# Kernel optimization log

Hardware: AMD Instinct MI355X
Metric: run time of the kernel (lower is better)

The kernel has to match this reference:

```python
import jax, jax.numpy as jnp
import numpy as np

N = 100000       # nodes
DEG = 16         # in-degree per node
E = N * DEG      # edges
IN_DIM = 128
H_DIM = 128
NEG_SLOPE = 0.01  # F.leaky_relu default


def setup_inputs() -> dict:
    key = jax.random.key(0)
    ks = jax.random.split(key, 12)
    sc = 0.05
    attr = jax.random.normal(ks[0], (N, IN_DIM), jnp.float32)
    edge_d = jax.random.uniform(ks[1], (E, 1), dtype=jnp.float32)
    edge_src = jax.random.randint(ks[2], (E,), 0, N, dtype=jnp.int32)
    edge_dst = jnp.repeat(jnp.arange(N, dtype=jnp.int32), DEG)  # every node gets DEG msgs
    return {
        "attr": attr,
        "edge_d": edge_d,
        "W_V1": jax.random.normal(ks[3], (1, 1), jnp.float32) * sc,
        "W_W1": jax.random.normal(ks[4], (H_DIM, IN_DIM), jnp.float32) * sc,
        "W_U1": jax.random.normal(ks[5], (H_DIM, IN_DIM), jnp.float32) * sc,
        "W_a1": jax.random.normal(ks[6], (1, 2 * H_DIM + 1), jnp.float32) * sc,
        "W_V2": jax.random.normal(ks[7], (1, 1), jnp.float32) * sc,
        "W_W2": jax.random.normal(ks[8], (H_DIM, H_DIM), jnp.float32) * sc,
        "W_U2": jax.random.normal(ks[9], (H_DIM, H_DIM), jnp.float32) * sc,
        "W_a2": jax.random.normal(ks[10], (1, 2 * H_DIM + 1), jnp.float32) * sc,
        "edge_src": edge_src,
        "edge_dst": edge_dst,
    }


def gat_layer(h, edge_d, edge_src, edge_dst, W_V, W_W, W_U, W_a):
    n = h.shape[0]
    t = edge_d @ W_V.T                      # [E,1] edge feature transform (fcV)
    z = h @ W_W.T                           # [N,H] (fcW)
    z_i = h @ W_U.T                         # [N,H] (fcU)
    Hd = z.shape[1]
    a = W_a[0]                              # [2H+1]
    a_src, a_dst, a_t = a[:Hd], a[Hd:2 * Hd], a[2 * Hd:]
    # attn_fc(concat(z_src, z_dst, t)) decomposed into per-node scores + edge term
    s_src = z @ a_src                       # [N]
    s_dst = z @ a_dst                       # [N]
    e = s_src[edge_src] + s_dst[edge_dst] + (t @ a_t)  # [E]
    e = jax.nn.leaky_relu(e, NEG_SLOPE)
    # per-destination-node softmax over incoming edges (mailbox softmax)
    m = jax.ops.segment_max(e, edge_dst, num_segments=n)
    ex = jnp.exp(e - m[edge_dst])
    denom = jax.ops.segment_sum(ex, edge_dst, num_segments=n)
    alpha = ex / denom[edge_dst]            # [E]
    # weighted neighbor aggregation
    zn = jax.ops.segment_sum(alpha[:, None] * z[edge_src], edge_dst, num_segments=n)
    return jax.nn.relu(z_i + zn)


def reference(attr, edge_d, W_V1, W_W1, W_U1, W_a1, W_V2, W_W2, W_U2, W_a2,
              edge_src, edge_dst):
    h = gat_layer(attr, edge_d, edge_src, edge_dst, W_V1, W_W1, W_U1, W_a1)
    h = gat_layer(h, edge_d, edge_src, edge_dst, W_V2, W_W2, W_U2, W_a2)
    return h
```

## Files before the change

### kernel.cpp

```cpp
#include <hip/hip_runtime.h>

#define N_NODES 100000
#define DEG 16
#define DIM 128
#define E_EDGES 1600000
#define NTILES 1563
#define T8 196
#define DGRID (T8 * 4 * 8)
#define LSTR 136

typedef short bf16x8 __attribute__((ext_vector_type(8)));
typedef float f32x4 __attribute__((ext_vector_type(4)));

__device__ __forceinline__ unsigned short f2bf(float f) {
    unsigned int u = __builtin_bit_cast(unsigned int, f);
    u = (u + 0x7fffu + ((u >> 16) & 1u)) >> 16;
    return (unsigned short)u;
}
__device__ __forceinline__ float bf2f(unsigned short h) {
    unsigned int u = ((unsigned int)h) << 16;
    return __builtin_bit_cast(float, u);
}
__device__ __forceinline__ bf16x8 pack_bf16x8(float4 lo, float4 hi) {
    bf16x8 f;
    f[0] = (short)f2bf(lo.x); f[1] = (short)f2bf(lo.y);
    f[2] = (short)f2bf(lo.z); f[3] = (short)f2bf(lo.w);
    f[4] = (short)f2bf(hi.x); f[5] = (short)f2bf(hi.y);
    f[6] = (short)f2bf(hi.z); f[7] = (short)f2bf(hi.w);
    return f;
}

__global__ __launch_bounds__(256) void prep_w(
    const float* __restrict__ W_W1, const float* __restrict__ W_U1,
    const float* __restrict__ W_W2, const float* __restrict__ W_U2,
    unsigned short* __restrict__ Wc1, unsigned short* __restrict__ Wc2)
{
    int idx = blockIdx.x * 256 + threadIdx.x;
    int half = idx & 32767;
    const float* src = (idx < 32768)
        ? (half < 16384 ? W_W1 + half : W_U1 + half - 16384)
        : (half < 16384 ? W_W2 + half : W_U2 + half - 16384);
    unsigned short* dst = (idx < 32768) ? Wc1 + half : Wc2 + half;
    *dst = f2bf(*src);
}

__global__ __launch_bounds__(256) void dense_tile(
    const float* __restrict__ hsrc,
    const unsigned short* __restrict__ Wc,
    const float* __restrict__ W_a,
    unsigned short* __restrict__ z,
    unsigned short* __restrict__ zi,
    float* __restrict__ s_src0, float* __restrict__ s_src1,
    float* __restrict__ s_dst0, float* __restrict__ s_dst1)
{
    __shared__ unsigned short Wt[64 * LSTR];
    __shared__ unsigned short Ht[64 * LSTR];

    const int bid = blockIdx.x;
    const int xcd = bid & 7;
    const int q = bid >> 3;
    const int cb = q & 3;
    const int tile = (q >> 2) * 8 + xcd;
    if (tile >= NTILES) return;
    const int nodebase = tile * 64;
    const int t = threadIdx.x;

    {
        int r = t >> 2, c0 = (t & 3) * 32;
        const unsigned short* src = Wc + (size_t)(cb * 64 + r) * DIM + c0;
        unsigned short* dst = Wt + r * LSTR + c0;
#pragma unroll
        for (int i = 0; i < 4; i++)
            *(uint4*)(dst + i * 8) = *(const uint4*)(src + i * 8);
    }
    {
        int r = t >> 2, c0 = (t & 3) * 32;
        int node = nodebase + r;
        unsigned short* dst = Ht + r * LSTR + c0;
        float4 v[8];
#pragma unroll
        for (int i = 0; i < 8; i++) v[i] = make_float4(0.f, 0.f, 0.f, 0.f);
        if (node < N_NODES) {
            const float* src = hsrc + (size_t)node * DIM + c0;
#pragma unroll
            for (int i = 0; i < 8; i++) v[i] = *(const float4*)(src + i * 4);
        }
#pragma unroll
        for (int i = 0; i < 4; i++)
            *(bf16x8*)(dst + i * 8) = pack_bf16x8(v[2 * i], v[2 * i + 1]);
    }
    __syncthreads();

    const int wave = t >> 6;
    const int lane = t & 63;
    const int n16 = lane & 15;
    const int quad = lane >> 4;
    const int node = nodebase + wave * 16 + n16;

    bf16x8 hfrag[4];
    const unsigned short* hrow = Ht + (wave * 16 + n16) * LSTR + quad * 8;
#pragma unroll
    for (int ks = 0; ks < 4; ks++)
        hfrag[ks] = *(const bf16x8*)(hrow + ks * 32);

    f32x4 acc[4];
#pragma unroll
    for (int ct = 0; ct < 4; ct++) {
        const unsigned short* wrow = Wt + (ct * 16 + n16) * LSTR + quad * 8;
        f32x4 a = {0.f, 0.f, 0.f, 0.f};
#pragma unroll
        for (int ks = 0; ks < 4; ks++)
            a = __builtin_amdgcn_mfma_f32_16x16x32_bf16(
                    *(const bf16x8*)(wrow + ks * 32), hfrag[ks], a, 0, 0, 0);
        acc[ct] = a;
    }

    if (node < N_NODES) {
        unsigned short* zout = (cb < 2 ? z : zi);
        unsigned short* orow = zout + (size_t)node * DIM + (cb & 1) * 64 + quad * 4;
#pragma unroll
        for (int ct = 0; ct < 4; ct++) {
            uint2 pk;
            pk.x = (unsigned int)f2bf(acc[ct][0]) | ((unsigned int)f2bf(acc[ct][1]) << 16);
            pk.y = (unsigned int)f2bf(acc[ct][2]) | ((unsigned int)f2bf(acc[ct][3]) << 16);
            *(uint2*)(orow + ct * 16) = pk;
        }
    }

    if (cb < 2) {
        float ps = 0.f, pd = 0.f;
#pragma unroll
        for (int ct = 0; ct < 4; ct++) {
            float4 as = *(const float4*)(W_a + cb * 64 + ct * 16 + quad * 4);
            float4 ad = *(const float4*)(W_a + DIM + cb * 64 + ct * 16 + quad * 4);
            ps += acc[ct][0] * as.x + acc[ct][1] * as.y
                + acc[ct][2] * as.z + acc[ct][3] * as.w;
            pd += acc[ct][0] * ad.x + acc[ct][1] * ad.y
                + acc[ct][2] * ad.z + acc[ct][3] * ad.w;
        }
        ps += __shfl_xor(ps, 16); ps += __shfl_xor(ps, 32);
        pd += __shfl_xor(pd, 16); pd += __shfl_xor(pd, 32);
        if (lane < 16 && node < N_NODES) {
            (cb == 0 ? s_src0 : s_src1)[node] = ps;
            (cb == 0 ? s_dst0 : s_dst1)[node] = pd;
        }
    }
}

__global__ __launch_bounds__(256) void dense_tile_b(
    const unsigned short* __restrict__ hsrc,
    const unsigned short* __restrict__ Wc,
    const float* __restrict__ W_a,
    unsigned short* __restrict__ z,
    unsigned short* __restrict__ zi,
    float* __restrict__ s_src0, float* __restrict__ s_src1,
    float* __restrict__ s_dst0, float* __restrict__ s_dst1)
{
    __shared__ unsigned short Wt[64 * LSTR];
    __shared__ unsigned short Ht[64 * LSTR];

    const int bid = blockIdx.x;
    const int xcd = bid & 7;
    const int q = bid >> 3;
    const int cb = q & 3;
    const int tile = (q >> 2) * 8 + xcd;
    if (tile >= NTILES) return;
    const int nodebase = tile * 64;
    const int t = threadIdx.x;

    {
        int r = t >> 2, c0 = (t & 3) * 32;
        const unsigned short* src = Wc + (size_t)(cb * 64 + r) * DIM + c0;
        unsigned short* dst = Wt + r * LSTR + c0;
#pragma unroll
        for (int i = 0; i < 4; i++)
            *(uint4*)(dst + i * 8) = *(const uint4*)(src + i * 8);
    }
    {
        int r = t >> 2, c0 = (t & 3) * 32;
        int node = nodebase + r;
        unsigned short* dst = Ht + r * LSTR + c0;
        if (node < N_NODES) {
            const unsigned short* src = hsrc + (size_t)node * DIM + c0;
#pragma unroll
            for (int i = 0; i < 4; i++)
                *(uint4*)(dst + i * 8) = *(const uint4*)(src + i * 8);
        } else {
            uint4 zr4 = make_uint4(0, 0, 0, 0);
#pragma unroll
            for (int i = 0; i < 4; i++) *(uint4*)(dst + i * 8) = zr4;
        }
    }
    __syncthreads();

    const int wave = t >> 6;
    const int lane = t & 63;
    const int n16 = lane & 15;
    const int quad = lane >> 4;
    const int node = nodebase + wave * 16 + n16;

    bf16x8 hfrag[4];
    const unsigned short* hrow = Ht + (wave * 16 + n16) * LSTR + quad * 8;
#pragma unroll
    for (int ks = 0; ks < 4; ks++)
        hfrag[ks] = *(const bf16x8*)(hrow + ks * 32);

    f32x4 acc[4];
#pragma unroll
    for (int ct = 0; ct < 4; ct++) {
        const unsigned short* wrow = Wt + (ct * 16 + n16) * LSTR + quad * 8;
        f32x4 a = {0.f, 0.f, 0.f, 0.f};
#pragma unroll
        for (int ks = 0; ks < 4; ks++)
            a = __builtin_amdgcn_mfma_f32_16x16x32_bf16(
                    *(const bf16x8*)(wrow + ks * 32), hfrag[ks], a, 0, 0, 0);
        acc[ct] = a;
    }

    if (node < N_NODES) {
        unsigned short* zout = (cb < 2 ? z : zi);
        unsigned short* orow = zout + (size_t)node * DIM + (cb & 1) * 64 + quad * 4;
#pragma unroll
        for (int ct = 0; ct < 4; ct++) {
            uint2 pk;
            pk.x = (unsigned int)f2bf(acc[ct][0]) | ((unsigned int)f2bf(acc[ct][1]) << 16);
            pk.y = (unsigned int)f2bf(acc[ct][2]) | ((unsigned int)f2bf(acc[ct][3]) << 16);
            *(uint2*)(orow + ct * 16) = pk;
        }
    }

    if (cb < 2) {
        float ps = 0.f, pd = 0.f;
#pragma unroll
        for (int ct = 0; ct < 4; ct++) {
            float4 as = *(const float4*)(W_a + cb * 64 + ct * 16 + quad * 4);
            float4 ad = *(const float4*)(W_a + DIM + cb * 64 + ct * 16 + quad * 4);
            ps += acc[ct][0] * as.x + acc[ct][1] * as.y
                + acc[ct][2] * as.z + acc[ct][3] * as.w;
            pd += acc[ct][0] * ad.x + acc[ct][1] * ad.y
                + acc[ct][2] * ad.z + acc[ct][3] * ad.w;
        }
        ps += __shfl_xor(ps, 16); ps += __shfl_xor(ps, 32);
        pd += __shfl_xor(pd, 16); pd += __shfl_xor(pd, 32);
        if (lane < 16 && node < N_NODES) {
            (cb == 0 ? s_src0 : s_src1)[node] = ps;
            (cb == 0 ? s_dst0 : s_dst1)[node] = pd;
        }
    }
}

__global__ __launch_bounds__(256) void alpha_k(
    const float* __restrict__ s_src0, const float* __restrict__ s_src1,
    const float* __restrict__ s_dst0, const float* __restrict__ s_dst1,
    const float* __restrict__ edge_d,
    const int* __restrict__ edge_src,
    const float* __restrict__ W_V,
    const float* __restrict__ W_a,
    float* __restrict__ alpha)
{
    const int e = blockIdx.x * 256 + threadIdx.x;
    const int node = e >> 4;
    int   s  = edge_src[e];
    float ed = edge_d[e];
    float coef = W_V[0] * W_a[2 * DIM];
    float x = (s_src0[s] + s_src1[s]) + (s_dst0[node] + s_dst1[node]) + ed * coef;
    x = x > 0.f ? x : 0.01f * x;
    float m = x;
    m = fmaxf(m, __shfl_xor(m, 1));
    m = fmaxf(m, __shfl_xor(m, 2));
    m = fmaxf(m, __shfl_xor(m, 4));
    m = fmaxf(m, __shfl_xor(m, 8));
    float ex = __expf(x - m);
    float d = ex;
    d += __shfl_xor(d, 1); d += __shfl_xor(d, 2);
    d += __shfl_xor(d, 4); d += __shfl_xor(d, 8);
    alpha[e] = ex / d;
}

__global__ __launch_bounds__(256) void aggr_row(
    const unsigned short* __restrict__ z,
    const unsigned short* __restrict__ zi,
    const float* __restrict__ alpha,
    const int* __restrict__ edge_src,
    unsigned short* __restrict__ hout)
{
    __shared__ float alpha_s[256];
    __shared__ int   src_s[256];

    const int t = threadIdx.x;
    const int base = blockIdx.x * 16;

    {
        int e0 = base * DEG + t;
        alpha_s[t] = alpha[e0];
        src_s[t]   = edge_src[e0];
    }
    __syncthreads();

    const int nl = t >> 4;
    const int j  = t & 15;
    const int node = base + nl;
    const int c8 = j * 8;
    const unsigned short* zc = z + c8;

    float acc[8] = {};
#pragma unroll
    for (int e = 0; e < DEG; e++) {
        int   sj = src_s[nl * 16 + e];
        float a  = alpha_s[nl * 16 + e];
        uint4 r = *(const uint4*)(zc + (size_t)sj * DIM);
        acc[0] += a * bf2f((unsigned short)(r.x & 0xffff));
        acc[1] += a * bf2f((unsigned short)(r.x >> 16));
        acc[2] += a * bf2f((unsigned short)(r.y & 0xffff));
        acc[3] += a * bf2f((unsigned short)(r.y >> 16));
        acc[4] += a * bf2f((unsigned short)(r.z & 0xffff));
        acc[5] += a * bf2f((unsigned short)(r.z >> 16));
        acc[6] += a * bf2f((unsigned short)(r.w & 0xffff));
        acc[7] += a * bf2f((unsigned short)(r.w >> 16));
    }

    uint4 zr = *(const uint4*)(zi + (size_t)node * DIM + c8);
    float v[8];
    v[0] = fmaxf(bf2f((unsigned short)(zr.x & 0xffff)) + acc[0], 0.f);
    v[1] = fmaxf(bf2f((unsigned short)(zr.x >> 16)) + acc[1], 0.f);
    v[2] = fmaxf(bf2f((unsigned short)(zr.y & 0xffff)) + acc[2], 0.f);
    v[3] = fmaxf(bf2f((unsigned short)(zr.y >> 16)) + acc[3], 0.f);
    v[4] = fmaxf(bf2f((unsigned short)(zr.z & 0xffff)) + acc[4], 0.f);
    v[5] = fmaxf(bf2f((unsigned short)(zr.z >> 16)) + acc[5], 0.f);
    v[6] = fmaxf(bf2f((unsigned short)(zr.w & 0xffff)) + acc[6], 0.f);
    v[7] = fmaxf(bf2f((unsigned short)(zr.w >> 16)) + acc[7], 0.f);

    uint4 pk;
    pk.x = (unsigned int)f2bf(v[0]) | ((unsigned int)f2bf(v[1]) << 16);
    pk.y = (unsigned int)f2bf(v[2]) | ((unsigned int)f2bf(v[3]) << 16);
    pk.z = (unsigned int)f2bf(v[4]) | ((unsigned int)f2bf(v[5]) << 16);
    pk.w = (unsigned int)f2bf(v[6]) | ((unsigned int)f2bf(v[7]) << 16);
    *(uint4*)(hout + (size_t)node * DIM + c8) = pk;
}

__global__ __launch_bounds__(256) void aggr_row_final(
    const unsigned short* __restrict__ z,
    const unsigned short* __restrict__ zi,
    const float* __restrict__ alpha,
    const int* __restrict__ edge_src,
    float* __restrict__ out_f32)
{
    __shared__ float alpha_s[256];
    __shared__ int   src_s[256];

    const int t = threadIdx.x;
    const int base = blockIdx.x * 16;

    {
        int e0 = base * DEG + t;
        alpha_s[t] = alpha[e0];
        src_s[t]   = edge_src[e0];
    }
    __syncthreads();

    const int nl = t >> 4;
    const int j  = t & 15;
    const int node = base + nl;
    const int c8 = j * 8;
    const unsigned short* zc = z + c8;

    float acc[8] = {};
#pragma unroll
    for (int e = 0; e < DEG; e++) {
        int   sj = src_s[nl * 16 + e];
        float a  = alpha_s[nl * 16 + e];
        uint4 r = *(const uint4*)(zc + (size_t)sj * DIM);
        acc[0] += a * bf2f((unsigned short)(r.x & 0xffff));
        acc[1] += a * bf2f((unsigned short)(r.x >> 16));
        acc[2] += a * bf2f((unsigned short)(r.y & 0xffff));
        acc[3] += a * bf2f((unsigned short)(r.y >> 16));
        acc[4] += a * bf2f((unsigned short)(r.z & 0xffff));
        acc[5] += a * bf2f((unsigned short)(r.z >> 16));
        acc[6] += a * bf2f((unsigned short)(r.w & 0xffff));
        acc[7] += a * bf2f((unsigned short)(r.w >> 16));
    }

    uint4 zr = *(const uint4*)(zi + (size_t)node * DIM + c8);
    float* op = out_f32 + (size_t)node * DIM + c8;
    f32x4 o0, o1;
    o0[0] = fmaxf(bf2f((unsigned short)(zr.x & 0xffff)) + acc[0], 0.f);
    o0[1] = fmaxf(bf2f((unsigned short)(zr.x >> 16)) + acc[1], 0.f);
    o0[2] = fmaxf(bf2f((unsigned short)(zr.y & 0xffff)) + acc[2], 0.f);
    o0[3] = fmaxf(bf2f((unsigned short)(zr.y >> 16)) + acc[3], 0.f);
    o1[0] = fmaxf(bf2f((unsigned short)(zr.z & 0xffff)) + acc[4], 0.f);
    o1[1] = fmaxf(bf2f((unsigned short)(zr.z >> 16)) + acc[5], 0.f);
    o1[2] = fmaxf(bf2f((unsigned short)(zr.w & 0xffff)) + acc[6], 0.f);
    o1[3] = fmaxf(bf2f((unsigned short)(zr.w >> 16)) + acc[7], 0.f);
    __builtin_nontemporal_store(o0, (f32x4*)op);
    __builtin_nontemporal_store(o1, (f32x4*)(op + 4));
}

extern "C" void kernel_launch(void* const* d_in, const int* in_sizes, int n_in,
                              void* d_out, int out_size, void* d_ws, size_t ws_size,
                              hipStream_t stream) {
    const float* attr     = (const float*)d_in[0];
    const float* edge_d   = (const float*)d_in[1];
    const float* W_V1     = (const float*)d_in[2];
    const float* W_W1     = (const float*)d_in[3];
    const float* W_U1     = (const float*)d_in[4];
    const float* W_a1     = (const float*)d_in[5];
    const float* W_V2     = (const float*)d_in[6];
    const float* W_W2     = (const float*)d_in[7];
    const float* W_U2     = (const float*)d_in[8];
    const float* W_a2     = (const float*)d_in[9];
    const int*   edge_src = (const int*)d_in[10];

    float* out = (float*)d_out;

    char* ws = (char*)d_ws;
    unsigned short* z1    = (unsigned short*)ws;
    unsigned short* zi1   = (unsigned short*)(ws + 26u * 1024 * 1024);
    unsigned short* h1    = (unsigned short*)(ws + 52u * 1024 * 1024);
    unsigned short* Wc1   = (unsigned short*)(ws + 78u * 1024 * 1024);
    unsigned short* Wc2   = (unsigned short*)(ws + 79u * 1024 * 1024);
    float* s_src0         = (float*)(ws + 80u * 1024 * 1024);
    float* s_src1         = (float*)(ws + 81u * 1024 * 1024);
    float* s_dst0         = (float*)(ws + 82u * 1024 * 1024);
    float* s_dst1         = (float*)(ws + 83u * 1024 * 1024);
    float* alphaA         = (float*)(ws + 84u * 1024 * 1024);
    unsigned short* z2  = z1;
    unsigned short* zi2 = zi1;

    prep_w<<<256, 256, 0, stream>>>(W_W1, W_U1, W_W2, W_U2, Wc1, Wc2);

    dense_tile<<<DGRID, 256, 0, stream>>>(attr, Wc1, W_a1, z1, zi1,
                                          s_src0, s_src1, s_dst0, s_dst1);

    alpha_k<<<6250, 256, 0, stream>>>(s_src0, s_src1, s_dst0, s_dst1,
                                      edge_d, edge_src, W_V1, W_a1, alphaA);

    aggr_row<<<6250, 256, 0, stream>>>(z1, zi1, alphaA, edge_src, h1);

    dense_tile_b<<<DGRID, 256, 0, stream>>>(h1, Wc2, W_a2, z2, zi2,
                                            s_src0, s_src1, s_dst0, s_dst1);

    alpha_k<<<6250, 256, 0, stream>>>(s_src0, s_src1, s_dst0, s_dst1,
                                      edge_d, edge_src, W_V2, W_a2, alphaA);

    aggr_row_final<<<6250, 256, 0, stream>>>(z2, zi2, alphaA, edge_src, out);
}
```

Before: 355.5 us.

## Fuse four column-block dense tiles per node tile, read weights directly from global

The dense kernels used to launch one block per (node tile, 64-column block), so each node tile's input rows were loaded and converted four times. Now one block per 64-node tile loads the input once into LDS and loops over all four column blocks. The weight tile is no longer staged in LDS and the MFMA operands are read straight from global memory (L1/L2 cached). This cuts the redundant activation reads, in particular the repeated fp32 loads of attr in layer 1. The cost is a grid about four times smaller, so less parallelism per kernel, and scattered global weight loads inside the MFMA loop.

```diff
diff --git a/kernel.cpp b/kernel.cpp
--- a/kernel.cpp
+++ b/kernel.cpp
@@ -5,8 +5,6 @@
 #define DIM 128
 #define E_EDGES 1600000
 #define NTILES 1563
-#define T8 196
-#define DGRID (T8 * 4 * 8)
 #define LSTR 136
 
 typedef short bf16x8 __attribute__((ext_vector_type(8)));
@@ -44,7 +42,7 @@
     *dst = f2bf(*src);
 }
 
-__global__ __launch_bounds__(256) void dense_tile(
+__global__ __launch_bounds__(256) void dense_fused(
     const float* __restrict__ hsrc,
     const unsigned short* __restrict__ Wc,
     const float* __restrict__ W_a,
@@ -53,26 +51,11 @@
     float* __restrict__ s_src0, float* __restrict__ s_src1,
     float* __restrict__ s_dst0, float* __restrict__ s_dst1)
 {
-    __shared__ unsigned short Wt[64 * LSTR];
     __shared__ unsigned short Ht[64 * LSTR];
 
-    const int bid = blockIdx.x;
-    const int xcd = bid & 7;
-    const int q = bid >> 3;
-    const int cb = q & 3;
-    const int tile = (q >> 2) * 8 + xcd;
-    if (tile >= NTILES) return;
-    const int nodebase = tile * 64;
+    const int nodebase = blockIdx.x * 64;
     const int t = threadIdx.x;
 
-    {
-        int r = t >> 2, c0 = (t & 3) * 32;
-        const unsigned short* src = Wc + (size_t)(cb * 64 + r) * DIM + c0;
-        unsigned short* dst = Wt + r * LSTR + c0;
-#pragma unroll
-        for (int i = 0; i < 4; i++)
-            *(uint4*)(dst + i * 8) = *(const uint4*)(src + i * 8);
-    }
     {
         int r = t >> 2, c0 = (t & 3) * 32;
         int node = nodebase + r;
@@ -103,51 +86,55 @@
     for (int ks = 0; ks < 4; ks++)
         hfrag[ks] = *(const bf16x8*)(hrow + ks * 32);
 
-    f32x4 acc[4];
-#pragma unroll
-    for (int ct = 0; ct < 4; ct++) {
-        const unsigned short* wrow = Wt + (ct * 16 + n16) * LSTR + quad * 8;
-        f32x4 a = {0.f, 0.f, 0.f, 0.f};
-#pragma unroll
-        for (int ks = 0; ks < 4; ks++)
-            a = __builtin_amdgcn_mfma_f32_16x16x32_bf16(
-                    *(const bf16x8*)(wrow + ks * 32), hfrag[ks], a, 0, 0, 0);
-        acc[ct] = a;
-    }
-
-    if (node < N_NODES) {
-        unsigned short* zout = (cb < 2 ? z : zi);
-        unsigned short* orow = zout + (size_t)node * DIM + (cb & 1) * 64 + quad * 4;
+#pragma unroll
+    for (int cb = 0; cb < 4; cb++) {
+        f32x4 acc[4];
 #pragma unroll
         for (int ct = 0; ct < 4; ct++) {
-            uint2 pk;
-            pk.x = (unsigned int)f2bf(acc[ct][0]) | ((unsigned int)f2bf(acc[ct][1]) << 16);
-            pk.y = (unsigned int)f2bf(acc[ct][2]) | ((unsigned int)f2bf(acc[ct][3]) << 16);
-            *(uint2*)(orow + ct * 16) = pk;
-        }
-    }
-
-    if (cb < 2) {
-        float ps = 0.f, pd = 0.f;
-#pragma unroll
-        for (int ct = 0; ct < 4; ct++) {
-            float4 as = *(const float4*)(W_a + cb * 64 + ct * 16 + quad * 4);
-            float4 ad = *(const float4*)(W_a + DIM + cb * 64 + ct * 16 + quad * 4);
-            ps += acc[ct][0] * as.x + acc[ct][1] * as.y
-                + acc[ct][2] * as.z + acc[ct][3] * as.w;
-            pd += acc[ct][0] * ad.x + acc[ct][1] * ad.y
-                + acc[ct][2] * ad.z + acc[ct][3] * ad.w;
-        }
-        ps += __shfl_xor(ps, 16); ps += __shfl_xor(ps, 32);
-        pd += __shfl_xor(pd, 16); pd += __shfl_xor(pd, 32);
-        if (lane < 16 && node < N_NODES) {
-            (cb == 0 ? s_src0 : s_src1)[node] = ps;
-            (cb == 0 ? s_dst0 : s_dst1)[node] = pd;
-        }
-    }
-}
-
-__global__ __launch_bounds__(256) void dense_tile_b(
+            const unsigned short* wrow =
+                Wc + (size_t)(cb * 64 + ct * 16 + n16) * DIM + quad * 8;
+            f32x4 a = {0.f, 0.f, 0.f, 0.f};
+#pragma unroll
+            for (int ks = 0; ks < 4; ks++)
+                a = __builtin_amdgcn_mfma_f32_16x16x32_bf16(
+                        *(const bf16x8*)(wrow + ks * 32), hfrag[ks], a, 0, 0, 0);
+            acc[ct] = a;
+        }
+
+        if (node < N_NODES) {
+            unsigned short* zout = (cb < 2 ? z : zi);
+            unsigned short* orow = zout + (size_t)node * DIM + (cb & 1) * 64 + quad * 4;
+#pragma unroll
+            for (int ct = 0; ct < 4; ct++) {
+                uint2 pk;
+                pk.x = (unsigned int)f2bf(acc[ct][0]) | ((unsigned int)f2bf(acc[ct][1]) << 16);
+                pk.y = (unsigned int)f2bf(acc[ct][2]) | ((unsigned int)f2bf(acc[ct][3]) << 16);
+                *(uint2*)(orow + ct * 16) = pk;
+            }
+        }
+
+        if (cb < 2) {
+            float ps = 0.f, pd = 0.f;
+#pragma unroll
+            for (int ct = 0; ct < 4; ct++) {
+                float4 as = *(const float4*)(W_a + cb * 64 + ct * 16 + quad * 4);
+                float4 ad = *(const float4*)(W_a + DIM + cb * 64 + ct * 16 + quad * 4);
+                ps += acc[ct][0] * as.x + acc[ct][1] * as.y
+                    + acc[ct][2] * as.z + acc[ct][3] * as.w;
+                pd += acc[ct][0] * ad.x + acc[ct][1] * ad.y
+                    + acc[ct][2] * ad.z + acc[ct][3] * ad.w;
+            }
+            ps += __shfl_xor(ps, 16); ps += __shfl_xor(ps, 32);
+            pd += __shfl_xor(pd, 16); pd += __shfl_xor(pd, 32);
+            if (lane < 16 && node < N_NODES) {
+                (cb == 0 ? s_src0 : s_src1)[node] = ps;
+                (cb == 0 ? s_dst0 : s_dst1)[node] = pd;
+            }
+        }
+    }
+}
+
+__global__ __launch_bounds__(256) void dense_fused_b(
     const unsigned short* __restrict__ hsrc,
     const unsigned short* __restrict__ Wc,
     const float* __restrict__ W_a,
@@ -156,26 +143,11 @@
     float* __restrict__ s_src0, float* __restrict__ s_src1,
     float* __restrict__ s_dst0, float* __restrict__ s_dst1)
 {
-    __shared__ unsigned short Wt[64 * LSTR];
     __shared__ unsigned short Ht[64 * LSTR];
 
-    const int bid = blockIdx.x;
-    const int xcd = bid & 7;
-    const int q = bid >> 3;
-    const int cb = q & 3;
-    const int tile = (q >> 2) * 8 + xcd;
-    if (tile >= NTILES) return;
-    const int nodebase = tile * 64;
+    const int nodebase = blockIdx.x * 64;
     const int t = threadIdx.x;
 
-    {
-        int r = t >> 2, c0 = (t & 3) * 32;
-        const unsigned short* src = Wc + (size_t)(cb * 64 + r) * DIM + c0;
-        unsigned short* dst = Wt + r * LSTR + c0;
-#pragma unroll
-        for (int i = 0; i < 4; i++)
-            *(uint4*)(dst + i * 8) = *(const uint4*)(src + i * 8);
-    }
     {
         int r = t >> 2, c0 = (t & 3) * 32;
         int node = nodebase + r;
@@ -205,46 +177,50 @@
     for (int ks = 0; ks < 4; ks++)
         hfrag[ks] = *(const bf16x8*)(hrow + ks * 32);
 
-    f32x4 acc[4];
-#pragma unroll
-    for (int ct = 0; ct < 4; ct++) {
-        const unsigned short* wrow = Wt + (ct * 16 + n16) * LSTR + quad * 8;
-        f32x4 a = {0.f, 0.f, 0.f, 0.f};
-#pragma unroll
-        for (int ks = 0; ks < 4; ks++)
-            a = __builtin_amdgcn_mfma_f32_16x16x32_bf16(
-                    *(const bf16x8*)(wrow + ks * 32), hfrag[ks], a, 0, 0, 0);
-        acc[ct] = a;
-    }
-
-    if (node < N_NODES) {
-        unsigned short* zout = (cb < 2 ? z : zi);
-        unsigned short* orow = zout + (size_t)node * DIM + (cb & 1) * 64 + quad * 4;
+#pragma unroll
+    for (int cb = 0; cb < 4; cb++) {
+        f32x4 acc[4];
 #pragma unroll
         for (int ct = 0; ct < 4; ct++) {
-            uint2 pk;
-            pk.x = (unsigned int)f2bf(acc[ct][0]) | ((unsigned int)f2bf(acc[ct][1]) << 16);
-            pk.y = (unsigned int)f2bf(acc[ct][2]) | ((unsigned int)f2bf(acc[ct][3]) << 16);
-            *(uint2*)(orow + ct * 16) = pk;
-        }
-    }
-
-    if (cb < 2) {
-        float ps = 0.f, pd = 0.f;
-#pragma unroll
-        for (int ct = 0; ct < 4; ct++) {
-            float4 as = *(const float4*)(W_a + cb * 64 + ct * 16 + quad * 4);
-            float4 ad = *(const float4*)(W_a + DIM + cb * 64 + ct * 16 + quad * 4);
-            ps += acc[ct][0] * as.x + acc[ct][1] * as.y
-                + acc[ct][2] * as.z + acc[ct][3] * as.w;
-            pd += acc[ct][0] * ad.x + acc[ct][1] * ad.y
-                + acc[ct][2] * ad.z + acc[ct][3] * ad.w;
-        }
-        ps += __shfl_xor(ps, 16); ps += __shfl_xor(ps, 32);
-        pd += __shfl_xor(pd, 16); pd += __shfl_xor(pd, 32);
-        if (lane < 16 && node < N_NODES) {
-            (cb == 0 ? s_src0 : s_src1)[node] = ps;
-            (cb == 0 ? s_dst0 : s_dst1)[node] = pd;
+            const unsigned short* wrow =
+                Wc + (size_t)(cb * 64 + ct * 16 + n16) * DIM + quad * 8;
+            f32x4 a = {0.f, 0.f, 0.f, 0.f};
+#pragma unroll
+            for (int ks = 0; ks < 4; ks++)
+                a = __builtin_amdgcn_mfma_f32_16x16x32_bf16(
+                        *(const bf16x8*)(wrow + ks * 32), hfrag[ks], a, 0, 0, 0);
+            acc[ct] = a;
+        }
+
+        if (node < N_NODES) {
+            unsigned short* zout = (cb < 2 ? z : zi);
+            unsigned short* orow = zout + (size_t)node * DIM + (cb & 1) * 64 + quad * 4;
+#pragma unroll
+            for (int ct = 0; ct < 4; ct++) {
+                uint2 pk;
+                pk.x = (unsigned int)f2bf(acc[ct][0]) | ((unsigned int)f2bf(acc[ct][1]) << 16);
+                pk.y = (unsigned int)f2bf(acc[ct][2]) | ((unsigned int)f2bf(acc[ct][3]) << 16);
+                *(uint2*)(orow + ct * 16) = pk;
+            }
+        }
+
+        if (cb < 2) {
+            float ps = 0.f, pd = 0.f;
+#pragma unroll
+            for (int ct = 0; ct < 4; ct++) {
+                float4 as = *(const float4*)(W_a + cb * 64 + ct * 16 + quad * 4);
+                float4 ad = *(const float4*)(W_a + DIM + cb * 64 + ct * 16 + quad * 4);
+                ps += acc[ct][0] * as.x + acc[ct][1] * as.y
+                    + acc[ct][2] * as.z + acc[ct][3] * as.w;
+                pd += acc[ct][0] * ad.x + acc[ct][1] * ad.y
+                    + acc[ct][2] * ad.z + acc[ct][3] * ad.w;
+            }
+            ps += __shfl_xor(ps, 16); ps += __shfl_xor(ps, 32);
+            pd += __shfl_xor(pd, 16); pd += __shfl_xor(pd, 32);
+            if (lane < 16 && node < N_NODES) {
+                (cb == 0 ? s_src0 : s_src1)[node] = ps;
+                (cb == 0 ? s_dst0 : s_dst1)[node] = pd;
+            }
         }
     }
 }
@@ -428,16 +404,16 @@
 
     prep_w<<<256, 256, 0, stream>>>(W_W1, W_U1, W_W2, W_U2, Wc1, Wc2);
 
-    dense_tile<<<DGRID, 256, 0, stream>>>(attr, Wc1, W_a1, z1, zi1,
-                                          s_src0, s_src1, s_dst0, s_dst1);
+    dense_fused<<<NTILES, 256, 0, stream>>>(attr, Wc1, W_a1, z1, zi1,
+                                            s_src0, s_src1, s_dst0, s_dst1);
 
     alpha_k<<<6250, 256, 0, stream>>>(s_src0, s_src1, s_dst0, s_dst1,
                                       edge_d, edge_src, W_V1, W_a1, alphaA);
 
     aggr_row<<<6250, 256, 0, stream>>>(z1, zi1, alphaA, edge_src, h1);
 
-    dense_tile_b<<<DGRID, 256, 0, stream>>>(h1, Wc2, W_a2, z2, zi2,
-                                            s_src0, s_src1, s_dst0, s_dst1);
+    dense_fused_b<<<NTILES, 256, 0, stream>>>(h1, Wc2, W_a2, z2, zi2,
+                                              s_src0, s_src1, s_dst0, s_dst1);
 
     alpha_k<<<6250, 256, 0, stream>>>(s_src0, s_src1, s_dst0, s_dst1,
                                       edge_d, edge_src, W_V2, W_a2, alphaA);
```

Result: slower. 409.7 us (+15.2%).
